# Optimization experiments

Measured on AMD Instinct MI355X. Metric: run time of the kernel, lower is better.

## Reference

```python
import jax, jax.numpy as jnp
import numpy as np

B, S, D, H = 8, 1300, 1080, 12
DK = D // H  # 90
FF = 3 * D   # 3240
EPS = 1e-5


def _layernorm(x, g, b):
    m = jnp.mean(x, axis=-1, keepdims=True)
    v = jnp.var(x, axis=-1, keepdims=True)
    return (x - m) * jax.lax.rsqrt(v + EPS) * g + b


def _rotate_half(x):
    x1, x2 = jnp.split(x, 2, axis=-1)
    return jnp.concatenate([-x2, x1], axis=-1)


def _rope(x, cos, sin):
    # x: [B,H,S,DK]; cos/sin: [S,DK] broadcast over batch/heads
    return x * cos + _rotate_half(x) * sin


def setup_inputs() -> dict:
    key = jax.random.key(0)
    ks = jax.random.split(key, 20)
    w = lambda k, sh: jax.random.normal(k, sh, dtype=jnp.float32) * 0.02
    inp = {
        'x': jax.random.normal(ks[0], (B, S, D), dtype=jnp.float32),
        'mask': jnp.tril(jnp.ones((S, S), dtype=jnp.int32))[None, None, :, :],
        'Wq': w(ks[1], (D, D)), 'bq': jnp.zeros((D,), jnp.float32),
        'Wk': w(ks[2], (D, D)), 'bk': jnp.zeros((D,), jnp.float32),
        'Wv': w(ks[3], (D, D)), 'bv': jnp.zeros((D,), jnp.float32),
        'Wo': w(ks[4], (D, D)), 'bo': jnp.zeros((D,), jnp.float32),
        'W1': w(ks[5], (D, FF)), 'b1': jnp.zeros((FF,), jnp.float32),
        'W2': w(ks[6], (FF, D)), 'b2': jnp.zeros((D,), jnp.float32),
        'W3': w(ks[7], (D, FF)), 'b3': jnp.zeros((FF,), jnp.float32),
        'ln1_g': jnp.ones((D,), jnp.float32), 'ln1_b': jnp.zeros((D,), jnp.float32),
        'ln2_g': jnp.ones((D,), jnp.float32), 'ln2_b': jnp.zeros((D,), jnp.float32),
    }
    # RoPE tables (buffers, not trainable)
    inv_freq = 1.0 / (10000.0 ** (jnp.arange(0, DK, 2, dtype=jnp.float32) / DK))
    t = jnp.arange(S, dtype=jnp.float32)
    freqs = t[:, None] * inv_freq[None, :]          # [S, DK/2]
    emb = jnp.concatenate([freqs, freqs], axis=-1)  # [S, DK]
    inp['rope_cos'] = jnp.cos(emb)
    inp['rope_sin'] = jnp.sin(emb)
    return inp


def reference(x, mask, Wq, bq, Wk, bk, Wv, bv, Wo, bo,
              W1, b1, W2, b2, W3, b3, ln1_g, ln1_b, ln2_g, ln2_b,
              rope_cos, rope_sin):
    # pre-norm attention block
    x2 = _layernorm(x, ln1_g, ln1_b)
    q = (x2 @ Wq + bq).reshape(B, S, H, DK).transpose(0, 2, 1, 3)  # [B,H,S,DK]
    k = (x2 @ Wk + bk).reshape(B, S, H, DK).transpose(0, 2, 1, 3)
    v = (x2 @ Wv + bv).reshape(B, S, H, DK).transpose(0, 2, 1, 3)
    q = _rope(q, rope_cos, rope_sin)
    k = _rope(k, rope_cos, rope_sin)
    scores = jnp.einsum('bhqd,bhkd->bhqk', q, k) / jnp.sqrt(jnp.float32(DK))
    scores = jnp.where(mask == 0, jnp.float32(-1e9), scores)
    p = jax.nn.softmax(scores, axis=-1)
    attn = jnp.einsum('bhqk,bhkd->bhqd', p, v)
    attn = attn.transpose(0, 2, 1, 3).reshape(B, S, D)
    x = x + (attn @ Wo + bo)
    # pre-norm SwiGLU FFN block
    x2 = _layernorm(x, ln2_g, ln2_b)
    h = jax.nn.silu(x2 @ W1 + b1) * (x2 @ W3 + b3)
    x = x + (h @ W2 + b2)
    return x
```

## Files before the change

### kernel.cpp

```cpp
#include <hip/hip_runtime.h>
#include <hip/hip_bf16.h>
#include <cstdint>
#include <cstddef>

#define B_  8
#define S_  1300
#define D_  1080
#define H_  12
#define DK_ 90
#define FF_ 3240
#define MROWS (B_*S_)
#define KP1 1088
#define KP2 3264
#define SP  1312
#define QKVN 3240
#define QSCALE 0.105409255338946f

typedef __hip_bfloat16 bf16;
typedef __bf16 bf16x8 __attribute__((ext_vector_type(8)));
typedef float  f32x4  __attribute__((ext_vector_type(4)));
typedef unsigned short u16x8 __attribute__((ext_vector_type(8)));

__device__ __forceinline__ void gload16(const void* g, void* l) {
    __builtin_amdgcn_global_load_lds((const __attribute__((address_space(1))) void*)g,
                                     (__attribute__((address_space(3))) void*)l, 16, 0, 0);
}
__device__ __forceinline__ unsigned short bf16bits(float f) {
    bf16 b = __float2bfloat16(f);
    return *(unsigned short*)&b;
}

__global__ __launch_bounds__(256) void zero_pads(bf16* __restrict__ buf)
{
    const int idx = blockIdx.x * 256 + threadIdx.x;
    if (idx >= MROWS * (KP1 - D_)) return;
    const int row = idx >> 3, col = D_ + (idx & 7);
    buf[(size_t)row * KP1 + col] = __float2bfloat16(0.f);
}

__global__ __launch_bounds__(256) void bcat(const float* __restrict__ bq,
    const float* __restrict__ bk, const float* __restrict__ bv,
    float* __restrict__ bqkv)
{
    const int i = blockIdx.x * 256 + threadIdx.x;
    if (i >= QKVN) return;
    bqkv[i] = (i < D_) ? bq[i] : (i < 2 * D_) ? bk[i - D_] : bv[i - 2 * D_];
}

__global__ __launch_bounds__(256) void castT(const float* __restrict__ W,
    bf16* __restrict__ WT, int K, int N, int KP)
{
    __shared__ unsigned short t[32][33];
    const int tx = threadIdx.x & 31, ty = threadIdx.x >> 5;
    const int k0 = blockIdx.x * 32, n0 = blockIdx.y * 32;
    #pragma unroll
    for (int i = 0; i < 4; ++i) {
        const int k = k0 + ty + 8 * i;
        const int n = n0 + tx;
        float v = (k < K && n < N) ? W[(size_t)k * N + n] : 0.f;
        t[ty + 8 * i][tx] = bf16bits(v);
    }
    __syncthreads();
    #pragma unroll
    for (int i = 0; i < 4; ++i) {
        const int n = n0 + ty + 8 * i;
        const int kk = k0 + tx;
        if (n < N && kk < KP) *(unsigned short*)&WT[(size_t)n * KP + kk] = t[tx][ty + 8 * i];
    }
}

__global__ __launch_bounds__(256) void ln_kernel(const float* __restrict__ x,
    const float* __restrict__ g, const float* __restrict__ b,
    bf16* __restrict__ y)
{
    __shared__ float xs[D_];
    __shared__ float red[8];
    const int row = blockIdx.x;
    const int tid = threadIdx.x;
    const float* xr = x + (size_t)row * D_;

    float s = 0.f, sq = 0.f;
    for (int d = tid; d < D_; d += 256) {
        float v = xr[d];
        xs[d] = v;
        s += v; sq += v * v;
    }
    #pragma unroll
    for (int off = 32; off > 0; off >>= 1) {
        s  += __shfl_down(s,  off, 64);
        sq += __shfl_down(sq, off, 64);
    }
    const int wave = tid >> 6, lane = tid & 63;
    if (lane == 0) { red[wave] = s; red[4 + wave] = sq; }
    __syncthreads();
    if (tid == 0) {
        float ts = 0.f, tq = 0.f;
        #pragma unroll
        for (int w = 0; w < 4; ++w) { ts += red[w]; tq += red[4 + w]; }
        red[0] = ts; red[4] = tq;
    }
    __syncthreads();
    const float mean = red[0] * (1.0f / D_);
    const float var  = red[4] * (1.0f / D_) - mean * mean;
    const float rstd = rsqrtf(var + 1e-5f);
    bf16* yr = y + (size_t)row * KP1;
    for (int d = tid; d < D_; d += 256)
        yr[d] = __float2bfloat16((xs[d] - mean) * rstd * g[d] + b[d]);
}

template<int MODE>
__global__ __launch_bounds__(256) void gemm_bf16(
    const bf16* __restrict__ A, const bf16* __restrict__ BT,
    const float* __restrict__ bias, const float* __restrict__ res,
    float* __restrict__ Cf, bf16* __restrict__ Cb,
    int M, int N, int KP, int LDC, int NP)
{
    __shared__ unsigned short As[128 * 32];
    __shared__ unsigned short Bs[128 * 32];

    const int tid = threadIdx.x;
    const int w = tid >> 6, l = tid & 63;
    const int m0 = blockIdx.y * 128, n0 = blockIdx.x * 128;

    const int rs = w * 16 + (l >> 2);
    const int kc = (l & 3) * 8;
    const int ar0 = min(m0 + rs,      M - 1);
    const int ar1 = min(m0 + rs + 64, M - 1);
    const int br0 = min(n0 + rs,      N - 1);
    const int br1 = min(n0 + rs + 64, N - 1);

    const int wm = (w >> 1) * 64, wn = (w & 1) * 64;
    const int lr = l & 15, kq = l >> 4;

    const unsigned short* aptr[4];
    const unsigned short* bptr[4];
    #pragma unroll
    for (int i = 0; i < 4; ++i) {
        aptr[i] = &As[(wm + i * 16 + lr) * 32 + kq * 8];
        bptr[i] = &Bs[(wn + i * 16 + lr) * 32 + kq * 8];
    }

    f32x4 acc[4][4] = {};

    const int nkt = KP >> 5;
    for (int kt = 0; kt < nkt; ++kt) {
        const int k0 = kt << 5;
        __syncthreads();
        gload16(A  + (size_t)ar0 * KP + k0 + kc, &As[w * 512]);
        gload16(A  + (size_t)ar1 * KP + k0 + kc, &As[2048 + w * 512]);
        gload16(BT + (size_t)br0 * KP + k0 + kc, &Bs[w * 512]);
        gload16(BT + (size_t)br1 * KP + k0 + kc, &Bs[2048 + w * 512]);
        __syncthreads();

        bf16x8 af[4], bv[4];
        #pragma unroll
        for (int i = 0; i < 4; ++i) af[i] = *(const bf16x8*)aptr[i];
        #pragma unroll
        for (int j = 0; j < 4; ++j) bv[j] = *(const bf16x8*)bptr[j];
        #pragma unroll
        for (int i = 0; i < 4; ++i)
            #pragma unroll
            for (int j = 0; j < 4; ++j)
                acc[i][j] = __builtin_amdgcn_mfma_f32_16x16x32_bf16(af[i], bv[j], acc[i][j], 0, 0, 0);
    }

    #pragma unroll
    for (int j = 0; j < 4; ++j) {
        const int n = n0 + wn + j * 16 + lr;
        if (n >= NP) continue;
        const bool real = (n < N);
        const float bn = real ? bias[n] : 0.f;
        #pragma unroll
        for (int i = 0; i < 4; ++i) {
            const int rowb = m0 + wm + i * 16 + kq * 4;
            #pragma unroll
            for (int r = 0; r < 4; ++r) {
                const int m = rowb + r;
                if (m < M) {
                    const size_t off = (size_t)m * LDC + n;
                    float val = acc[i][j][r] + bn;
                    if (MODE == 0) Cf[off] = val;
                    if (MODE == 1) Cf[off] = val + res[off];
                    if (MODE == 3) Cb[off] = real ? __float2bfloat16(val) : __float2bfloat16(0.f);
                    if (MODE == 2) {
                        if (real) {
                            const float prev = __bfloat162float(Cb[off]);
                            const float sig  = 1.0f / (1.0f + __expf(-prev));
                            Cb[off] = __float2bfloat16(prev * sig * val);
                        } else {
                            Cb[off] = __float2bfloat16(0.f);
                        }
                    }
                }
            }
        }
    }
}

__global__ __launch_bounds__(256) void rope_qk(const bf16* __restrict__ qkv,
    const float* __restrict__ cosb, const float* __restrict__ sinb,
    bf16* __restrict__ Qa, bf16* __restrict__ Ka)
{
    const int s = blockIdx.x;
    const int b = blockIdx.y;
    const int tid = threadIdx.x;

    if (s >= S_) {
        for (int idx = tid; idx < H_ * 96; idx += 256) {
            const int h = idx / 96, c = idx - (idx / 96) * 96;
            const size_t o = ((size_t)(b * H_ + h) * SP + s) * 96 + c;
            Qa[o] = __float2bfloat16(0.f);
            Ka[o] = __float2bfloat16(0.f);
        }
        return;
    }

    const bf16* row = qkv + (size_t)(b * S_ + s) * QKVN;

    for (int idx = tid; idx < H_ * 45; idx += 256) {
        const int h = idx / 45, d = idx - (idx / 45) * 45;
        const float c1 = cosb[s * DK_ + d],      s1 = sinb[s * DK_ + d];
        const float c2 = cosb[s * DK_ + d + 45], s2 = sinb[s * DK_ + d + 45];
        const size_t o = ((size_t)(b * H_ + h) * SP + s) * 96;
        const float q1 = __bfloat162float(row[h * DK_ + d]);
        const float q2 = __bfloat162float(row[h * DK_ + d + 45]);
        Qa[o + d]      = __float2bfloat16((q1 * c1 - q2 * s1) * QSCALE);
        Qa[o + d + 45] = __float2bfloat16((q2 * c2 + q1 * s2) * QSCALE);
        const float k1 = __bfloat162float(row[D_ + h * DK_ + d]);
        const float k2 = __bfloat162float(row[D_ + h * DK_ + d + 45]);
        Ka[o + d]      = __float2bfloat16(k1 * c1 - k2 * s1);
        Ka[o + d + 45] = __float2bfloat16(k2 * c2 + k1 * s2);
    }
    for (int idx = tid; idx < H_ * 6; idx += 256) {
        const int h = idx / 6, c = 90 + (idx - (idx / 6) * 6);
        const size_t o = ((size_t)(b * H_ + h) * SP + s) * 96 + c;
        Qa[o] = __float2bfloat16(0.f);
        Ka[o] = __float2bfloat16(0.f);
    }
}

__global__ __launch_bounds__(256) void vtrans(const bf16* __restrict__ qkv,
    bf16* __restrict__ Vt)
{
    __shared__ float T[96][33];
    const int k0 = blockIdx.x * 32;
    const int bh = blockIdx.y;
    const int b = bh / H_, h = bh % H_;
    const int tid = threadIdx.x;

    for (int idx = tid; idx < 32 * 90; idx += 256) {
        const int r = idx / 90, d = idx - (idx / 90) * 90;
        const int s = k0 + r;
        T[d][r] = (s < S_) ?
            __bfloat162float(qkv[(size_t)(b * S_ + s) * QKVN + 2 * D_ + h * DK_ + d]) : 0.f;
    }
    for (int idx = tid; idx < 32 * 6; idx += 256) {
        const int r = idx / 6, d = 90 + (idx - (idx / 6) * 6);
        T[d][r] = 0.f;
    }
    __syncthreads();
    for (int idx = tid; idx < 96 * 4; idx += 256) {
        const int d = idx >> 2, kk = (idx & 3) * 8;
        u16x8 v;
        #pragma unroll
        for (int i = 0; i < 8; ++i) v[i] = bf16bits(T[d][kk + i]);
        *(u16x8*)(Vt + ((size_t)bh * 96 + d) * SP + k0 + kk) = v;
    }
}

__global__ __launch_bounds__(256) void attn_mfma(const bf16* __restrict__ Qa,
    const bf16* __restrict__ Ka, const bf16* __restrict__ Vt,
    bf16* __restrict__ ab)
{
    __shared__ unsigned short Qs[64][104];
    __shared__ unsigned short Ks[32][104];
    __shared__ unsigned short Vs[96][40];
    __shared__ unsigned short Ps[4][16][40];

    const int tid = threadIdx.x;
    const int w = tid >> 6, l = tid & 63;
    const int lr = l & 15, kq = l >> 4;
    const int qblk = (int)gridDim.x - 1 - (int)blockIdx.x;
    const int q0 = qblk * 64;
    const int bh = blockIdx.y;
    const int b = bh / H_, h = bh % H_;

    const bf16* Qg = Qa + (size_t)bh * SP * 96;
    const bf16* Kg = Ka + (size_t)bh * SP * 96;
    const bf16* Vg = Vt + (size_t)bh * 96 * SP;

    for (int c = tid; c < 768; c += 256) {
        const int row = c / 12, cc = c - row * 12;
        const int rg = q0 + row;
        u16x8 v = (u16x8)0;
        if (rg < SP) v = *(const u16x8*)(Qg + (size_t)rg * 96 + cc * 8);
        *(u16x8*)&Qs[row][cc * 8] = v;
    }
    __syncthreads();

    bf16x8 Qf[3];
    #pragma unroll
    for (int kf = 0; kf < 3; ++kf)
        Qf[kf] = *(const bf16x8*)&Qs[w * 16 + lr][kf * 32 + kq * 8];

    const int qw0 = q0 + w * 16;
    const int myq = qw0 + lr;
    const int wlq = (qw0 < S_) ? min(qw0 + 15, S_ - 1) : -1;
    const int lastq = min(q0 + 63, S_ - 1);
    const int ntiles = lastq / 32 + 1;

    f32x4 Of[6] = {};
    float mrun = -1e30f, lrun = 0.f;

    for (int kt = 0; kt < ntiles; ++kt) {
        const int k0 = kt * 32;
        __syncthreads();
        for (int c = tid; c < 384; c += 256) {
            const int row = c / 12, cc = c - (c / 12) * 12;
            *(u16x8*)&Ks[row][cc * 8] = *(const u16x8*)(Kg + (size_t)(k0 + row) * 96 + cc * 8);
        }
        for (int c = tid; c < 384; c += 256) {
            const int d = c >> 2, kk = (c & 3) * 8;
            *(u16x8*)&Vs[d][kk] = *(const u16x8*)(Vg + (size_t)d * SP + k0 + kk);
        }
        __syncthreads();

        if (k0 > wlq) continue;

        f32x4 sg0 = {0.f, 0.f, 0.f, 0.f}, sg1 = {0.f, 0.f, 0.f, 0.f};
        #pragma unroll
        for (int kf = 0; kf < 3; ++kf) {
            bf16x8 k0f = *(const bf16x8*)&Ks[lr][kf * 32 + kq * 8];
            bf16x8 k1f = *(const bf16x8*)&Ks[16 + lr][kf * 32 + kq * 8];
            sg0 = __builtin_amdgcn_mfma_f32_16x16x32_bf16(k0f, Qf[kf], sg0, 0, 0, 0);
            sg1 = __builtin_amdgcn_mfma_f32_16x16x32_bf16(k1f, Qf[kf], sg1, 0, 0, 0);
        }

        float e[8];
        float msub = -1e30f;
        #pragma unroll
        for (int r = 0; r < 4; ++r) {
            const int ka = k0 + 4 * kq + r;
            const int kb = ka + 16;
            const float a = (ka <= myq && ka < S_) ? sg0[r] : -1e30f;
            const float c = (kb <= myq && kb < S_) ? sg1[r] : -1e30f;
            e[r] = a; e[4 + r] = c;
            msub = fmaxf(msub, fmaxf(a, c));
        }
        msub = fmaxf(msub, __shfl_xor(msub, 16, 64));
        msub = fmaxf(msub, __shfl_xor(msub, 32, 64));
        const float nm = fmaxf(mrun, msub);
        const float resc = __expf(mrun - nm);
        mrun = nm;
        float ls = 0.f;
        #pragma unroll
        for (int i = 0; i < 8; ++i) {
            const float ev = (e[i] > -1e29f) ? __expf(e[i] - nm) : 0.f;
            e[i] = ev; ls += ev;
        }
        ls += __shfl_xor(ls, 16, 64);
        ls += __shfl_xor(ls, 32, 64);
        lrun = lrun * resc + ls;

        ushort4 p0, p1;
        p0.x = bf16bits(e[0]); p0.y = bf16bits(e[1]); p0.z = bf16bits(e[2]); p0.w = bf16bits(e[3]);
        p1.x = bf16bits(e[4]); p1.y = bf16bits(e[5]); p1.z = bf16bits(e[6]); p1.w = bf16bits(e[7]);
        *(ushort4*)&Ps[w][lr][4 * kq]      = p0;
        *(ushort4*)&Ps[w][lr][16 + 4 * kq] = p1;

        float rf[4];
        #pragma unroll
        for (int r = 0; r < 4; ++r) rf[r] = __shfl(resc, 4 * kq + r, 16);
        #pragma unroll
        for (int c = 0; c < 6; ++c)
            #pragma unroll
            for (int r = 0; r < 4; ++r)
                Of[c][r] *= rf[r];

        bf16x8 Pf = *(const bf16x8*)&Ps[w][lr][kq * 8];
        #pragma unroll
        for (int c = 0; c < 6; ++c) {
            bf16x8 Vf = *(const bf16x8*)&Vs[16 * c + lr][kq * 8];
            Of[c] = __builtin_amdgcn_mfma_f32_16x16x32_bf16(Pf, Vf, Of[c], 0, 0, 0);
        }
    }

    const float invq = 1.0f / lrun;
    float inv[4];
    #pragma unroll
    for (int r = 0; r < 4; ++r) inv[r] = __shfl(invq, 4 * kq + r, 16);
    #pragma unroll
    for (int c = 0; c < 6; ++c) {
        const int dim = 16 * c + lr;
        if (dim >= DK_) continue;
        #pragma unroll
        for (int r = 0; r < 4; ++r) {
            const int qrow = qw0 + 4 * kq + r;
            if (qrow < S_)
                ab[(size_t)(b * S_ + qrow) * KP1 + h * DK_ + dim] =
                    __float2bfloat16(Of[c][r] * inv[r]);
        }
    }
}

extern "C" void kernel_launch(void* const* d_in, const int* in_sizes, int n_in,
                              void* d_out, int out_size, void* d_ws, size_t ws_size,
                              hipStream_t stream)
{
    const float* x    = (const float*)d_in[0];
    const float* Wq   = (const float*)d_in[2];
    const float* bq   = (const float*)d_in[3];
    const float* Wk   = (const float*)d_in[4];
    const float* bk   = (const float*)d_in[5];
    const float* Wv   = (const float*)d_in[6];
    const float* bv   = (const float*)d_in[7];
    const float* Wo   = (const float*)d_in[8];
    const float* bo   = (const float*)d_in[9];
    const float* W1   = (const float*)d_in[10];
    const float* b1   = (const float*)d_in[11];
    const float* W2   = (const float*)d_in[12];
    const float* b2   = (const float*)d_in[13];
    const float* W3   = (const float*)d_in[14];
    const float* b3   = (const float*)d_in[15];
    const float* ln1g = (const float*)d_in[16];
    const float* ln1b = (const float*)d_in[17];
    const float* ln2g = (const float*)d_in[18];
    const float* ln2b = (const float*)d_in[19];
    const float* rc   = (const float*)d_in[20];
    const float* rs   = (const float*)d_in[21];
    float* out = (float*)d_out;

    char* wsb = (char*)d_ws;
    size_t off = 0;
    auto nxt = [&](size_t bytes) -> char* {
        char* p = wsb + off; off += (bytes + 255) & ~(size_t)255; return p;
    };
    bf16*  x2   = (bf16*)nxt((size_t)MROWS * KP1 * 2);
    bf16*  qkv  = (bf16*)nxt((size_t)MROWS * KP2 * 2);
    float* x1f  = (float*)nxt((size_t)MROWS * D_ * 4);
    bf16*  ab   = (bf16*)nxt((size_t)MROWS * KP1 * 2);
    bf16*  WqkvT= (bf16*)nxt((size_t)QKVN * KP1 * 2);
    bf16*  WoT  = (bf16*)nxt((size_t)D_ * KP1 * 2);
    bf16*  W1T  = (bf16*)nxt((size_t)FF_ * KP1 * 2);
    bf16*  W3T  = (bf16*)nxt((size_t)FF_ * KP1 * 2);
    bf16*  W2T  = (bf16*)nxt((size_t)D_ * KP2 * 2);
    bf16*  Qa   = (bf16*)nxt((size_t)B_ * H_ * SP * 96 * 2);
    bf16*  Ka   = (bf16*)nxt((size_t)B_ * H_ * SP * 96 * 2);
    float* bqkv = (float*)nxt((size_t)QKVN * 4);
    bf16*  Vt   = (bf16*)x1f;
    float* x1   = x1f;
    bf16*  hb   = qkv;

    const dim3 blk(256);
    const dim3 gD(9, 82);
    const dim3 gF(26, 82);
    const int padN = MROWS * (KP1 - D_);

    zero_pads<<<(padN + 255) / 256, blk, 0, stream>>>(x2);
    zero_pads<<<(padN + 255) / 256, blk, 0, stream>>>(ab);
    bcat<<<(QKVN + 255) / 256, blk, 0, stream>>>(bq, bk, bv, bqkv);

    castT<<<dim3(34, 34),  blk, 0, stream>>>(Wq, WqkvT,                    D_, D_, KP1);
    castT<<<dim3(34, 34),  blk, 0, stream>>>(Wk, WqkvT + (size_t)D_ * KP1, D_, D_, KP1);
    castT<<<dim3(34, 34),  blk, 0, stream>>>(Wv, WqkvT + (size_t)2*D_*KP1, D_, D_, KP1);
    castT<<<dim3(34, 34),  blk, 0, stream>>>(Wo, WoT, D_, D_, KP1);
    castT<<<dim3(34, 102), blk, 0, stream>>>(W1, W1T, D_, FF_, KP1);
    castT<<<dim3(34, 102), blk, 0, stream>>>(W3, W3T, D_, FF_, KP1);
    castT<<<dim3(102, 34), blk, 0, stream>>>(W2, W2T, FF_, D_, KP2);

    ln_kernel<<<MROWS, blk, 0, stream>>>(x, ln1g, ln1b, x2);
    gemm_bf16<3><<<gF, blk, 0, stream>>>(x2, WqkvT, bqkv, nullptr, nullptr, qkv,
                                         MROWS, QKVN, KP1, QKVN, QKVN);
    rope_qk<<<dim3(SP, B_), blk, 0, stream>>>(qkv, rc, rs, Qa, Ka);
    vtrans<<<dim3(41, B_ * H_), blk, 0, stream>>>(qkv, Vt);
    attn_mfma<<<dim3(21, B_ * H_), blk, 0, stream>>>(Qa, Ka, Vt, ab);
    gemm_bf16<1><<<gD, blk, 0, stream>>>(ab, WoT, bo, x, x1, nullptr, MROWS, D_, KP1, D_, D_);
    ln_kernel<<<MROWS, blk, 0, stream>>>(x1, ln2g, ln2b, x2);
    gemm_bf16<3><<<gF, blk, 0, stream>>>(x2, W1T, b1, nullptr, nullptr, hb, MROWS, FF_, KP1, KP2, KP2);
    gemm_bf16<2><<<gF, blk, 0, stream>>>(x2, W3T, b3, nullptr, nullptr, hb, MROWS, FF_, KP1, KP2, KP2);
    gemm_bf16<1><<<gD, blk, 0, stream>>>(hb, W2T, b2, x1, out, nullptr, MROWS, D_, KP2, D_, D_);
}
```

Measured before the change: 1.144 ms.

## Replace 128x128 GEMM with 256x256 tile, 4-stage LDS pipeline and swizzle

```diff
diff --git a/kernel.cpp b/kernel.cpp
--- a/kernel.cpp
+++ b/kernel.cpp
@@ -109,59 +109,99 @@
 }
 
 template<int MODE>
-__global__ __launch_bounds__(256) void gemm_bf16(
+__global__ __launch_bounds__(512, 2) void gemm256(
     const bf16* __restrict__ A, const bf16* __restrict__ BT,
     const float* __restrict__ bias, const float* __restrict__ res,
     float* __restrict__ Cf, bf16* __restrict__ Cb,
-    int M, int N, int KP, int LDC, int NP)
-{
-    __shared__ unsigned short As[128 * 32];
-    __shared__ unsigned short Bs[128 * 32];
+    int M, int N, int KP, int LDC, int NP, int NT)
+{
+    __shared__ unsigned short lds[65536];
 
     const int tid = threadIdx.x;
     const int w = tid >> 6, l = tid & 63;
-    const int m0 = blockIdx.y * 128, n0 = blockIdx.x * 128;
-
-    const int rs = w * 16 + (l >> 2);
-    const int kc = (l & 3) * 8;
-    const int ar0 = min(m0 + rs,      M - 1);
-    const int ar1 = min(m0 + rs + 64, M - 1);
-    const int br0 = min(n0 + rs,      N - 1);
-    const int br1 = min(n0 + rs + 64, N - 1);
-
-    const int wm = (w >> 1) * 64, wn = (w & 1) * 64;
     const int lr = l & 15, kq = l >> 4;
-
-    const unsigned short* aptr[4];
-    const unsigned short* bptr[4];
-    #pragma unroll
-    for (int i = 0; i < 4; ++i) {
-        aptr[i] = &As[(wm + i * 16 + lr) * 32 + kq * 8];
-        bptr[i] = &Bs[(wn + i * 16 + lr) * 32 + kq * 8];
-    }
-
-    f32x4 acc[4][4] = {};
-
-    const int nkt = KP >> 5;
-    for (int kt = 0; kt < nkt; ++kt) {
-        const int k0 = kt << 5;
-        __syncthreads();
-        gload16(A  + (size_t)ar0 * KP + k0 + kc, &As[w * 512]);
-        gload16(A  + (size_t)ar1 * KP + k0 + kc, &As[2048 + w * 512]);
-        gload16(BT + (size_t)br0 * KP + k0 + kc, &Bs[w * 512]);
-        gload16(BT + (size_t)br1 * KP + k0 + kc, &Bs[2048 + w * 512]);
-        __syncthreads();
+    const int wm = (w >> 2) * 128;
+    const int wn = (w & 3) * 64;
+    const int m0 = blockIdx.y * 256, n0 = blockIdx.x * 256;
+
+    const int cof = (kq ^ ((lr >> 1) & 3)) << 3;
+    const int aro = (wm + lr) * 32 + cof;
+    const int bro = 8192 + (wn + lr) * 32 + cof;
+
+    const int srow = tid >> 2;
+    const int sch  = (tid & 3) ^ ((srow >> 1) & 3);
+    const int ar0 = min(m0 + srow,       M - 1);
+    const int ar1 = min(m0 + 128 + srow, M - 1);
+    const int br0 = min(n0 + srow,       N - 1);
+    const int br1 = min(n0 + 128 + srow, N - 1);
+    const bf16* ag0 = A  + (size_t)ar0 * KP + sch * 8;
+    const bf16* ag1 = A  + (size_t)ar1 * KP + sch * 8;
+    const bf16* bg0 = BT + (size_t)br0 * KP + sch * 8;
+    const bf16* bg1 = BT + (size_t)br1 * KP + sch * 8;
+    const int wds = w * 512;
+
+    f32x4 acc[8][4] = {};
+
+    #pragma unroll
+    for (int tt = 0; tt < 3; ++tt) {
+        const int so = tt * 16384;
+        const int kn = tt * 32;
+        gload16(ag0 + kn, &lds[so + wds]);
+        gload16(ag1 + kn, &lds[so + 4096  + wds]);
+        gload16(bg0 + kn, &lds[so + 8192  + wds]);
+        gload16(bg1 + kn, &lds[so + 12288 + wds]);
+    }
+    asm volatile("s_waitcnt vmcnt(8)" ::: "memory");
+    __builtin_amdgcn_s_barrier();
+
+    for (int t = 0; t < NT; ++t) {
+        const unsigned short* sl = &lds[(t & 3) * 16384];
+        const unsigned short* pa = sl + aro;
+        const unsigned short* pb = sl + bro;
+        const int so = ((t + 3) & 3) * 16384;
+        const int kn = (t + 3) * 32;
+        const bool st = (t + 3) < NT;
 
         bf16x8 af[4], bv[4];
         #pragma unroll
-        for (int i = 0; i < 4; ++i) af[i] = *(const bf16x8*)aptr[i];
-        #pragma unroll
-        for (int j = 0; j < 4; ++j) bv[j] = *(const bf16x8*)bptr[j];
+        for (int i = 0; i < 4; ++i) af[i] = *(const bf16x8*)(pa + i * 512);
+        #pragma unroll
+        for (int j = 0; j < 4; ++j) bv[j] = *(const bf16x8*)(pb + j * 512);
+        if (st) {
+            gload16(ag0 + kn, &lds[so + wds]);
+            gload16(ag1 + kn, &lds[so + 4096 + wds]);
+        }
+        __builtin_amdgcn_s_barrier();
+        asm volatile("s_waitcnt lgkmcnt(0)" ::: "memory");
+        __builtin_amdgcn_s_setprio(1);
         #pragma unroll
         for (int i = 0; i < 4; ++i)
             #pragma unroll
             for (int j = 0; j < 4; ++j)
                 acc[i][j] = __builtin_amdgcn_mfma_f32_16x16x32_bf16(af[i], bv[j], acc[i][j], 0, 0, 0);
+        __builtin_amdgcn_s_setprio(0);
+        __builtin_amdgcn_s_barrier();
+
+        bf16x8 af2[4];
+        #pragma unroll
+        for (int i = 0; i < 4; ++i) af2[i] = *(const bf16x8*)(pa + (4 + i) * 512);
+        if (st) {
+            gload16(bg0 + kn, &lds[so + 8192  + wds]);
+            gload16(bg1 + kn, &lds[so + 12288 + wds]);
+        }
+        if (t < NT - 3)       { asm volatile("s_waitcnt vmcnt(8)" ::: "memory"); }
+        else if (t == NT - 3) { asm volatile("s_waitcnt vmcnt(4)" ::: "memory"); }
+        else if (t == NT - 2) { asm volatile("s_waitcnt vmcnt(0)" ::: "memory"); }
+        __builtin_amdgcn_s_barrier();
+        asm volatile("s_waitcnt lgkmcnt(0)" ::: "memory");
+        __builtin_amdgcn_s_setprio(1);
+        #pragma unroll
+        for (int i = 0; i < 4; ++i)
+            #pragma unroll
+            for (int j = 0; j < 4; ++j)
+                acc[4 + i][j] = __builtin_amdgcn_mfma_f32_16x16x32_bf16(af2[i], bv[j], acc[4 + i][j], 0, 0, 0);
+        __builtin_amdgcn_s_setprio(0);
+        __builtin_amdgcn_s_barrier();
     }
 
     #pragma unroll
@@ -171,7 +211,7 @@
         const bool real = (n < N);
         const float bn = real ? bias[n] : 0.f;
         #pragma unroll
-        for (int i = 0; i < 4; ++i) {
+        for (int i = 0; i < 8; ++i) {
             const int rowb = m0 + wm + i * 16 + kq * 4;
             #pragma unroll
             for (int r = 0; r < 4; ++r) {
@@ -452,8 +492,9 @@
     bf16*  hb   = qkv;
 
     const dim3 blk(256);
-    const dim3 gD(9, 82);
-    const dim3 gF(26, 82);
+    const dim3 blk5(512);
+    const dim3 g256F(13, 41);
+    const dim3 g256D(5, 41);
     const int padN = MROWS * (KP1 - D_);
 
     zero_pads<<<(padN + 255) / 256, blk, 0, stream>>>(x2);
@@ -469,14 +510,18 @@
     castT<<<dim3(102, 34), blk, 0, stream>>>(W2, W2T, FF_, D_, KP2);
 
     ln_kernel<<<MROWS, blk, 0, stream>>>(x, ln1g, ln1b, x2);
-    gemm_bf16<3><<<gF, blk, 0, stream>>>(x2, WqkvT, bqkv, nullptr, nullptr, qkv,
-                                         MROWS, QKVN, KP1, QKVN, QKVN);
+    gemm256<3><<<g256F, blk5, 0, stream>>>(x2, WqkvT, bqkv, nullptr, nullptr, qkv,
+                                           MROWS, QKVN, KP1, QKVN, QKVN, KP1 / 32);
     rope_qk<<<dim3(SP, B_), blk, 0, stream>>>(qkv, rc, rs, Qa, Ka);
     vtrans<<<dim3(41, B_ * H_), blk, 0, stream>>>(qkv, Vt);
     attn_mfma<<<dim3(21, B_ * H_), blk, 0, stream>>>(Qa, Ka, Vt, ab);
-    gemm_bf16<1><<<gD, blk, 0, stream>>>(ab, WoT, bo, x, x1, nullptr, MROWS, D_, KP1, D_, D_);
+    gemm256<1><<<g256D, blk5, 0, stream>>>(ab, WoT, bo, x, x1, nullptr,
+                                           MROWS, D_, KP1, D_, D_, KP1 / 32);
     ln_kernel<<<MROWS, blk, 0, stream>>>(x1, ln2g, ln2b, x2);
-    gemm_bf16<3><<<gF, blk, 0, stream>>>(x2, W1T, b1, nullptr, nullptr, hb, MROWS, FF_, KP1, KP2, KP2);
-    gemm_bf16<2><<<gF, blk, 0, stream>>>(x2, W3T, b3, nullptr, nullptr, hb, MROWS, FF_, KP1, KP2, KP2);
-    gemm_bf16<1><<<gD, blk, 0, stream>>>(hb, W2T, b2, x1, out, nullptr, MROWS, D_, KP2, D_, D_);
-}
+    gemm256<3><<<g256F, blk5, 0, stream>>>(x2, W1T, b1, nullptr, nullptr, hb,
+                                           MROWS, FF_, KP1, KP2, KP2, KP1 / 32);
+    gemm256<2><<<g256F, blk5, 0, stream>>>(x2, W3T, b3, nullptr, nullptr, hb,
+                                           MROWS, FF_, KP1, KP2, KP2, KP1 / 32);
+    gemm256<1><<<g256D, blk5, 0, stream>>>(hb, W2T, b2, x1, out, nullptr,
+                                           MROWS, D_, KP2, D_, D_, KP2 / 32);
+}
```

Measured after the change: 1.244 ms. 8.8% more time.

## Replace GEMM with 256x256 double-buffered swizzled-LDS kernel and XCD remap

Applied to the files above, without the earlier changes.

```diff
diff --git a/kernel.cpp b/kernel.cpp
--- a/kernel.cpp
+++ b/kernel.cpp
@@ -10,8 +10,8 @@
 #define DK_ 90
 #define FF_ 3240
 #define MROWS (B_*S_)
-#define KP1 1088
-#define KP2 3264
+#define KP1 1152
+#define KP2 3328
 #define SP  1312
 #define QKVN 3240
 #define QSCALE 0.105409255338946f
@@ -20,6 +20,7 @@
 typedef __bf16 bf16x8 __attribute__((ext_vector_type(8)));
 typedef float  f32x4  __attribute__((ext_vector_type(4)));
 typedef unsigned short u16x8 __attribute__((ext_vector_type(8)));
+typedef unsigned int   u32x4 __attribute__((ext_vector_type(4)));
 
 __device__ __forceinline__ void gload16(const void* g, void* l) {
     __builtin_amdgcn_global_load_lds((const __attribute__((address_space(1))) void*)g,
@@ -29,12 +30,24 @@
     bf16 b = __float2bfloat16(f);
     return *(unsigned short*)&b;
 }
+__device__ __forceinline__ bf16x8 dsr(unsigned byteaddr) {
+    union { u32x4 u; bf16x8 b; } c;
+    asm volatile("ds_read_b128 %0, %1" : "=&v"(c.u) : "v"(byteaddr));
+    return c.b;
+}
+
+#define BAR()   __builtin_amdgcn_s_barrier()
+#define LGKM0() asm volatile("s_waitcnt lgkmcnt(0)" ::: "memory")
+#define VMC4()  asm volatile("s_waitcnt vmcnt(4)" ::: "memory")
+#define VMC0()  asm volatile("s_waitcnt vmcnt(0)" ::: "memory")
+#define SCB()   __builtin_amdgcn_sched_barrier(0)
 
 __global__ __launch_bounds__(256) void zero_pads(bf16* __restrict__ buf)
 {
+    const int PADC = KP1 - D_;
     const int idx = blockIdx.x * 256 + threadIdx.x;
-    if (idx >= MROWS * (KP1 - D_)) return;
-    const int row = idx >> 3, col = D_ + (idx & 7);
+    if (idx >= MROWS * PADC) return;
+    const int row = idx / PADC, col = D_ + (idx - row * PADC);
     buf[(size_t)row * KP1 + col] = __float2bfloat16(0.f);
 }
 
@@ -109,60 +122,141 @@
 }
 
 template<int MODE>
-__global__ __launch_bounds__(256) void gemm_bf16(
+__global__ __launch_bounds__(512, 2) void gemm256(
     const bf16* __restrict__ A, const bf16* __restrict__ BT,
     const float* __restrict__ bias, const float* __restrict__ res,
     float* __restrict__ Cf, bf16* __restrict__ Cb,
-    int M, int N, int KP, int LDC, int NP)
-{
-    __shared__ unsigned short As[128 * 32];
-    __shared__ unsigned short Bs[128 * 32];
+    int M, int N, int KP, int LDC, int NP, int NI)
+{
+    __shared__ unsigned short lds[65536];
 
     const int tid = threadIdx.x;
     const int w = tid >> 6, l = tid & 63;
-    const int m0 = blockIdx.y * 128, n0 = blockIdx.x * 128;
-
-    const int rs = w * 16 + (l >> 2);
-    const int kc = (l & 3) * 8;
-    const int ar0 = min(m0 + rs,      M - 1);
-    const int ar1 = min(m0 + rs + 64, M - 1);
-    const int br0 = min(n0 + rs,      N - 1);
-    const int br1 = min(n0 + rs + 64, N - 1);
-
-    const int wm = (w >> 1) * 64, wn = (w & 1) * 64;
     const int lr = l & 15, kq = l >> 4;
-
-    const unsigned short* aptr[4];
-    const unsigned short* bptr[4];
-    #pragma unroll
-    for (int i = 0; i < 4; ++i) {
-        aptr[i] = &As[(wm + i * 16 + lr) * 32 + kq * 8];
-        bptr[i] = &Bs[(wn + i * 16 + lr) * 32 + kq * 8];
-    }
-
-    f32x4 acc[4][4] = {};
-
-    const int nkt = KP >> 5;
-    for (int kt = 0; kt < nkt; ++kt) {
-        const int k0 = kt << 5;
-        __syncthreads();
-        gload16(A  + (size_t)ar0 * KP + k0 + kc, &As[w * 512]);
-        gload16(A  + (size_t)ar1 * KP + k0 + kc, &As[2048 + w * 512]);
-        gload16(BT + (size_t)br0 * KP + k0 + kc, &Bs[w * 512]);
-        gload16(BT + (size_t)br1 * KP + k0 + kc, &Bs[2048 + w * 512]);
-        __syncthreads();
-
-        bf16x8 af[4], bv[4];
-        #pragma unroll
-        for (int i = 0; i < 4; ++i) af[i] = *(const bf16x8*)aptr[i];
-        #pragma unroll
-        for (int j = 0; j < 4; ++j) bv[j] = *(const bf16x8*)bptr[j];
-        #pragma unroll
-        for (int i = 0; i < 4; ++i)
-            #pragma unroll
-            for (int j = 0; j < 4; ++j)
-                acc[i][j] = __builtin_amdgcn_mfma_f32_16x16x32_bf16(af[i], bv[j], acc[i][j], 0, 0, 0);
-    }
+    const int wm = (w >> 2) * 128;
+    const int wn = (w & 3) * 64;
+    const int NT = NI * 2;
+
+    int wg = blockIdx.y * (int)gridDim.x + blockIdx.x;
+    const int nwg = (int)gridDim.x * (int)gridDim.y;
+    const int q8 = nwg >> 3, r8 = nwg & 7;
+    const int xcd = wg & 7, lot = wg >> 3;
+    wg = (xcd < r8 ? xcd * (q8 + 1) : r8 * (q8 + 1) + (xcd - r8) * q8) + lot;
+    const int m0 = (wg / (int)gridDim.x) * 256;
+    const int n0 = (wg % (int)gridDim.x) * 256;
+
+    const unsigned ldsb = (unsigned)(size_t)(const __attribute__((address_space(3))) void*)&lds[0];
+    const int axr = lr & 7;
+    const unsigned co0 = (unsigned)((kq       ^ axr) * 16);
+    const unsigned co1 = (unsigned)(((4 + kq) ^ axr) * 16);
+    const unsigned ldsA = ldsb + (unsigned)((wm + lr) * 128);
+    const unsigned ldsB = ldsb + 65536u + (unsigned)((wn + lr) * 128);
+
+    const int srow8 = tid >> 3, sc = tid & 7;
+    const int sx = ((sc ^ (srow8 & 7)) * 8);
+    const bf16* pA[4]; const bf16* pB[4];
+    #pragma unroll
+    for (int q = 0; q < 4; ++q) {
+        pA[q] = A  + (size_t)min(m0 + q * 64 + srow8, M - 1) * KP + sx;
+        pB[q] = BT + (size_t)min(n0 + q * 64 + srow8, N - 1) * KP + sx;
+    }
+    const int wds = w * 512;
+
+#define STG(P, q, tile, baseS) gload16((P)[q] + (size_t)(tile) * 64, &lds[(baseS) + (q) * 4096 + wds])
+
+#define RDA(bufb, mh) do { \
+    const unsigned _ab = ldsA + (bufb) + (mh) * 8192; \
+    afr[0][0] = dsr(_ab +    0 + co0); afr[0][1] = dsr(_ab +    0 + co1); \
+    afr[1][0] = dsr(_ab + 2048 + co0); afr[1][1] = dsr(_ab + 2048 + co1); \
+    afr[2][0] = dsr(_ab + 4096 + co0); afr[2][1] = dsr(_ab + 4096 + co1); \
+    afr[3][0] = dsr(_ab + 6144 + co0); afr[3][1] = dsr(_ab + 6144 + co1); \
+} while (0)
+
+#define RDB(bufb, nh) do { \
+    const unsigned _bb = ldsB + (bufb) + (nh) * 4096; \
+    bfr[(nh)*2    ][0] = dsr(_bb +    0 + co0); bfr[(nh)*2    ][1] = dsr(_bb +    0 + co1); \
+    bfr[(nh)*2 + 1][0] = dsr(_bb + 2048 + co0); bfr[(nh)*2 + 1][1] = dsr(_bb + 2048 + co1); \
+} while (0)
+
+#define MFQ(ai, jb) do { \
+    _Pragma("unroll") \
+    for (int i_ = 0; i_ < 4; ++i_) { \
+        _Pragma("unroll") \
+        for (int jj_ = 0; jj_ < 2; ++jj_) { \
+            acc[(ai)+i_][(jb)+jj_] = __builtin_amdgcn_mfma_f32_16x16x32_bf16(afr[i_][0], bfr[(jb)+jj_][0], acc[(ai)+i_][(jb)+jj_], 0, 0, 0); \
+            acc[(ai)+i_][(jb)+jj_] = __builtin_amdgcn_mfma_f32_16x16x32_bf16(afr[i_][1], bfr[(jb)+jj_][1], acc[(ai)+i_][(jb)+jj_], 0, 0, 0); \
+        } } } while (0)
+
+    f32x4 acc[8][4] = {};
+    bf16x8 afr[4][2], bfr[4][2];
+
+    STG(pA, 0, 0, 0);     STG(pA, 2, 0, 0);
+    STG(pA, 1, 0, 0);     STG(pA, 3, 0, 0);
+    STG(pB, 0, 0, 32768); STG(pB, 1, 0, 32768);
+    STG(pB, 2, 0, 32768); STG(pB, 3, 0, 32768);
+    STG(pB, 0, 1, 49152); STG(pB, 1, 1, 49152);
+    STG(pB, 2, 1, 49152); STG(pB, 3, 1, 49152);
+    VMC4();
+    BAR();
+
+    for (int it = 0; it < NI; ++it) {
+        const int c1 = 2 * it + 1, u0 = 2 * it + 2, u1 = 2 * it + 3;
+        const bool g0 = u0 < NT, g1 = u1 < NT;
+        const bool lastit = (it == NI - 1);
+
+        RDA(0, 0); RDB(0, 0);
+        STG(pA, 0, c1, 16384); STG(pA, 2, c1, 16384);
+        BAR(); LGKM0(); SCB();
+        __builtin_amdgcn_s_setprio(1); MFQ(0, 0); __builtin_amdgcn_s_setprio(0);
+        SCB(); BAR();
+
+        RDB(0, 1);
+        STG(pA, 1, c1, 16384); STG(pA, 3, c1, 16384);
+        BAR(); LGKM0(); SCB();
+        __builtin_amdgcn_s_setprio(1); MFQ(0, 2); __builtin_amdgcn_s_setprio(0);
+        SCB(); BAR();
+
+        RDA(0, 1);
+        if (g0) { STG(pA, 0, u0, 0); STG(pA, 2, u0, 0); }
+        BAR(); LGKM0(); SCB();
+        __builtin_amdgcn_s_setprio(1); MFQ(4, 2); __builtin_amdgcn_s_setprio(0);
+        SCB(); BAR();
+
+        if (g0) { STG(pA, 1, u0, 0); STG(pA, 3, u0, 0); }
+        if (lastit) { VMC0(); } else { VMC4(); }
+        BAR(); SCB();
+        __builtin_amdgcn_s_setprio(1); MFQ(4, 0); __builtin_amdgcn_s_setprio(0);
+        SCB(); BAR();
+
+        RDA(32768, 0); RDB(32768, 0);
+        if (g0) { STG(pB, 0, u0, 32768); STG(pB, 1, u0, 32768); }
+        BAR(); LGKM0(); SCB();
+        __builtin_amdgcn_s_setprio(1); MFQ(0, 0); __builtin_amdgcn_s_setprio(0);
+        SCB(); BAR();
+
+        RDB(32768, 1);
+        if (g0) { STG(pB, 2, u0, 32768); STG(pB, 3, u0, 32768); }
+        BAR(); LGKM0(); SCB();
+        __builtin_amdgcn_s_setprio(1); MFQ(0, 2); __builtin_amdgcn_s_setprio(0);
+        SCB(); BAR();
+
+        RDA(32768, 1);
+        if (g1) { STG(pB, 0, u1, 49152); STG(pB, 1, u1, 49152); }
+        BAR(); LGKM0(); SCB();
+        __builtin_amdgcn_s_setprio(1); MFQ(4, 2); __builtin_amdgcn_s_setprio(0);
+        SCB(); BAR();
+
+        if (g1) { STG(pB, 2, u1, 49152); STG(pB, 3, u1, 49152); }
+        VMC4();
+        BAR(); SCB();
+        __builtin_amdgcn_s_setprio(1); MFQ(4, 0); __builtin_amdgcn_s_setprio(0);
+        SCB(); BAR();
+    }
+
+#undef STG
+#undef RDA
+#undef RDB
+#undef MFQ
 
     #pragma unroll
     for (int j = 0; j < 4; ++j) {
@@ -171,7 +265,7 @@
         const bool real = (n < N);
         const float bn = real ? bias[n] : 0.f;
         #pragma unroll
-        for (int i = 0; i < 4; ++i) {
+        for (int i = 0; i < 8; ++i) {
             const int rowb = m0 + wm + i * 16 + kq * 4;
             #pragma unroll
             for (int r = 0; r < 4; ++r) {
@@ -452,31 +546,36 @@
     bf16*  hb   = qkv;
 
     const dim3 blk(256);
-    const dim3 gD(9, 82);
-    const dim3 gF(26, 82);
+    const dim3 blk5(512);
+    const dim3 g256F(13, 41);
+    const dim3 g256D(5, 41);
     const int padN = MROWS * (KP1 - D_);
 
     zero_pads<<<(padN + 255) / 256, blk, 0, stream>>>(x2);
     zero_pads<<<(padN + 255) / 256, blk, 0, stream>>>(ab);
     bcat<<<(QKVN + 255) / 256, blk, 0, stream>>>(bq, bk, bv, bqkv);
 
-    castT<<<dim3(34, 34),  blk, 0, stream>>>(Wq, WqkvT,                    D_, D_, KP1);
-    castT<<<dim3(34, 34),  blk, 0, stream>>>(Wk, WqkvT + (size_t)D_ * KP1, D_, D_, KP1);
-    castT<<<dim3(34, 34),  blk, 0, stream>>>(Wv, WqkvT + (size_t)2*D_*KP1, D_, D_, KP1);
-    castT<<<dim3(34, 34),  blk, 0, stream>>>(Wo, WoT, D_, D_, KP1);
-    castT<<<dim3(34, 102), blk, 0, stream>>>(W1, W1T, D_, FF_, KP1);
-    castT<<<dim3(34, 102), blk, 0, stream>>>(W3, W3T, D_, FF_, KP1);
-    castT<<<dim3(102, 34), blk, 0, stream>>>(W2, W2T, FF_, D_, KP2);
+    castT<<<dim3(36, 34),  blk, 0, stream>>>(Wq, WqkvT,                    D_, D_, KP1);
+    castT<<<dim3(36, 34),  blk, 0, stream>>>(Wk, WqkvT + (size_t)D_ * KP1, D_, D_, KP1);
+    castT<<<dim3(36, 34),  blk, 0, stream>>>(Wv, WqkvT + (size_t)2*D_*KP1, D_, D_, KP1);
+    castT<<<dim3(36, 34),  blk, 0, stream>>>(Wo, WoT, D_, D_, KP1);
+    castT<<<dim3(36, 102), blk, 0, stream>>>(W1, W1T, D_, FF_, KP1);
+    castT<<<dim3(36, 102), blk, 0, stream>>>(W3, W3T, D_, FF_, KP1);
+    castT<<<dim3(104, 34), blk, 0, stream>>>(W2, W2T, FF_, D_, KP2);
 
     ln_kernel<<<MROWS, blk, 0, stream>>>(x, ln1g, ln1b, x2);
-    gemm_bf16<3><<<gF, blk, 0, stream>>>(x2, WqkvT, bqkv, nullptr, nullptr, qkv,
-                                         MROWS, QKVN, KP1, QKVN, QKVN);
+    gemm256<3><<<g256F, blk5, 0, stream>>>(x2, WqkvT, bqkv, nullptr, nullptr, qkv,
+                                           MROWS, QKVN, KP1, QKVN, QKVN, KP1 / 128);
     rope_qk<<<dim3(SP, B_), blk, 0, stream>>>(qkv, rc, rs, Qa, Ka);
     vtrans<<<dim3(41, B_ * H_), blk, 0, stream>>>(qkv, Vt);
     attn_mfma<<<dim3(21, B_ * H_), blk, 0, stream>>>(Qa, Ka, Vt, ab);
-    gemm_bf16<1><<<gD, blk, 0, stream>>>(ab, WoT, bo, x, x1, nullptr, MROWS, D_, KP1, D_, D_);
+    gemm256<1><<<g256D, blk5, 0, stream>>>(ab, WoT, bo, x, x1, nullptr,
+                                           MROWS, D_, KP1, D_, D_, KP1 / 128);
     ln_kernel<<<MROWS, blk, 0, stream>>>(x1, ln2g, ln2b, x2);
-    gemm_bf16<3><<<gF, blk, 0, stream>>>(x2, W1T, b1, nullptr, nullptr, hb, MROWS, FF_, KP1, KP2, KP2);
-    gemm_bf16<2><<<gF, blk, 0, stream>>>(x2, W3T, b3, nullptr, nullptr, hb, MROWS, FF_, KP1, KP2, KP2);
-    gemm_bf16<1><<<gD, blk, 0, stream>>>(hb, W2T, b2, x1, out, nullptr, MROWS, D_, KP2, D_, D_);
-}
+    gemm256<3><<<g256F, blk5, 0, stream>>>(x2, W1T, b1, nullptr, nullptr, hb,
+                                           MROWS, FF_, KP1, KP2, KP2, KP1 / 128);
+    gemm256<2><<<g256F, blk5, 0, stream>>>(x2, W3T, b3, nullptr, nullptr, hb,
+                                           MROWS, FF_, KP1, KP2, KP2, KP1 / 128);
+    gemm256<1><<<g256D, blk5, 0, stream>>>(hb, W2T, b2, x1, out, nullptr,
+                                           MROWS, D_, KP2, D_, D_, KP2 / 128);
+}
```

New measurement: 1.399 ms. 1.22x slower.

## Double-buffer GEMM LDS tiles and remap workgroups across XCDs

Applied to the files above, without the earlier changes.

```diff
diff --git a/kernel.cpp b/kernel.cpp
--- a/kernel.cpp
+++ b/kernel.cpp
@@ -115,12 +115,19 @@
     float* __restrict__ Cf, bf16* __restrict__ Cb,
     int M, int N, int KP, int LDC, int NP)
 {
-    __shared__ unsigned short As[128 * 32];
-    __shared__ unsigned short Bs[128 * 32];
+    __shared__ unsigned short As[2 * 128 * 32];
+    __shared__ unsigned short Bs[2 * 128 * 32];
 
     const int tid = threadIdx.x;
     const int w = tid >> 6, l = tid & 63;
-    const int m0 = blockIdx.y * 128, n0 = blockIdx.x * 128;
+
+    int wg = blockIdx.y * (int)gridDim.x + blockIdx.x;
+    const int nwg = (int)gridDim.x * (int)gridDim.y;
+    const int q8 = nwg >> 3, r8 = nwg & 7;
+    const int xcd = wg & 7, lot = wg >> 3;
+    wg = (xcd < r8 ? xcd * (q8 + 1) : r8 * (q8 + 1) + (xcd - r8) * q8) + lot;
+    const int m0 = (wg % (int)gridDim.x) * 128;
+    const int n0 = (wg / (int)gridDim.x) * 128;
 
     const int rs = w * 16 + (l >> 2);
     const int kc = (l & 3) * 8;
@@ -132,36 +139,50 @@
     const int wm = (w >> 1) * 64, wn = (w & 1) * 64;
     const int lr = l & 15, kq = l >> 4;
 
-    const unsigned short* aptr[4];
-    const unsigned short* bptr[4];
+    int aoff[4], boff[4];
     #pragma unroll
     for (int i = 0; i < 4; ++i) {
-        aptr[i] = &As[(wm + i * 16 + lr) * 32 + kq * 8];
-        bptr[i] = &Bs[(wn + i * 16 + lr) * 32 + kq * 8];
+        aoff[i] = (wm + i * 16 + lr) * 32 + kq * 8;
+        boff[i] = (wn + i * 16 + lr) * 32 + kq * 8;
     }
 
     f32x4 acc[4][4] = {};
-
     const int nkt = KP >> 5;
+
+    {
+        gload16(A  + (size_t)ar0 * KP + kc, &As[w * 512]);
+        gload16(A  + (size_t)ar1 * KP + kc, &As[2048 + w * 512]);
+        gload16(BT + (size_t)br0 * KP + kc, &Bs[w * 512]);
+        gload16(BT + (size_t)br1 * KP + kc, &Bs[2048 + w * 512]);
+    }
+    __syncthreads();
+
+    int cur = 0;
     for (int kt = 0; kt < nkt; ++kt) {
-        const int k0 = kt << 5;
-        __syncthreads();
-        gload16(A  + (size_t)ar0 * KP + k0 + kc, &As[w * 512]);
-        gload16(A  + (size_t)ar1 * KP + k0 + kc, &As[2048 + w * 512]);
-        gload16(BT + (size_t)br0 * KP + k0 + kc, &Bs[w * 512]);
-        gload16(BT + (size_t)br1 * KP + k0 + kc, &Bs[2048 + w * 512]);
-        __syncthreads();
-
+        if (kt + 1 < nkt) {
+            const int kn = (kt + 1) << 5;
+            const int nb = (cur ^ 1) * 4096;
+            gload16(A  + (size_t)ar0 * KP + kn + kc, &As[nb + w * 512]);
+            gload16(A  + (size_t)ar1 * KP + kn + kc, &As[nb + 2048 + w * 512]);
+            gload16(BT + (size_t)br0 * KP + kn + kc, &Bs[nb + w * 512]);
+            gload16(BT + (size_t)br1 * KP + kn + kc, &Bs[nb + 2048 + w * 512]);
+        }
+
+        const unsigned short* ab = &As[cur * 4096];
+        const unsigned short* bb = &Bs[cur * 4096];
         bf16x8 af[4], bv[4];
         #pragma unroll
-        for (int i = 0; i < 4; ++i) af[i] = *(const bf16x8*)aptr[i];
-        #pragma unroll
-        for (int j = 0; j < 4; ++j) bv[j] = *(const bf16x8*)bptr[j];
+        for (int i = 0; i < 4; ++i) af[i] = *(const bf16x8*)(ab + aoff[i]);
+        #pragma unroll
+        for (int j = 0; j < 4; ++j) bv[j] = *(const bf16x8*)(bb + boff[j]);
         #pragma unroll
         for (int i = 0; i < 4; ++i)
             #pragma unroll
             for (int j = 0; j < 4; ++j)
                 acc[i][j] = __builtin_amdgcn_mfma_f32_16x16x32_bf16(af[i], bv[j], acc[i][j], 0, 0, 0);
+
+        __syncthreads();
+        cur ^= 1;
     }
 
     #pragma unroll
@@ -452,8 +473,8 @@
     bf16*  hb   = qkv;
 
     const dim3 blk(256);
-    const dim3 gD(9, 82);
-    const dim3 gF(26, 82);
+    const dim3 gF(82, 26);
+    const dim3 gD(82, 9);
     const int padN = MROWS * (KP1 - D_);
 
     zero_pads<<<(padN + 255) / 256, blk, 0, stream>>>(x2);
```

Result: no change. 1.133 ms (-0.9%).
